# Performance work log

Measured on AMD Instinct MI355X. Metric: run time of the kernel, lower is better.

## Reference

```python
import jax, jax.numpy as jnp
import numpy as np

D = 1024  # encoder_output_size

def setup_inputs() -> dict:
    key = jax.random.key(0)
    ks = jax.random.split(key, 5)
    scale = 1.0 / np.sqrt(D)  # roughly matches nn.Linear init spread
    seq = jax.random.normal(ks[0], (2048, 8, D), dtype=jnp.float32)
    Kw1 = jax.random.normal(ks[1], (D, D), dtype=jnp.float32) * scale
    Kw2 = jax.random.normal(ks[2], (D, D), dtype=jnp.float32) * scale
    Qw1 = jax.random.normal(ks[3], (D, D), dtype=jnp.float32) * scale
    Qw2 = jax.random.normal(ks[4], (D, D), dtype=jnp.float32) * scale
    return {"sequence": seq, "Kw1": Kw1, "Kw2": Kw2, "Qw1": Qw1, "Qw2": Qw2}

def _mlp(x, W1, W2):
    # nn.Linear(bias=False): y = x @ W^T ; tanh after each
    return jnp.tanh(jnp.tanh(x @ W1.T) @ W2.T)

def reference(sequence, Kw1, Kw2, Qw1, Qw2):
    x = jnp.transpose(sequence, (1, 0, 2))          # [B, S, D]
    keys = _mlp(x, Kw1, Kw2)                        # [B, S, D]
    queries = _mlp(x, Qw1, Qw2)                     # [B, S, D]
    scale = 1.0 / jnp.sqrt(jnp.float32(x.shape[-1]))
    weights = jnp.einsum('bsd,btd->bst', keys, queries) * scale  # [B, S, S]
    weights = jax.nn.softmax(weights, axis=-1)
    attended = jnp.einsum('bst,btd->bsd', weights, x)            # [B, S, D]
    return jnp.transpose(attended, (1, 0, 2))       # [S, B, D]
```

## Files before the change

kernel.cpp:

```cpp
#include <hip/hip_runtime.h>
#include <hip/hip_bf16.h>

#define SEQ 2048
#define NB 8
#define DIM 1024

typedef __attribute__((ext_vector_type(4))) float f32x4;
typedef __attribute__((ext_vector_type(8))) short bf16x8;
typedef __attribute__((ext_vector_type(4))) unsigned short u16x4;

__device__ __forceinline__ unsigned short f2bf(float f) {
    union { float f; unsigned u; } x; x.f = f;
    unsigned r = x.u + 0x7fffu + ((x.u >> 16) & 1u);
    return (unsigned short)(r >> 16);
}
__device__ __forceinline__ float bf2f(unsigned short u) {
    union { unsigned u; float f; } x; x.u = ((unsigned)u) << 16;
    return x.f;
}

__global__ __launch_bounds__(256) void convert_w4(const float* __restrict__ s0,
                                                  const float* __restrict__ s1,
                                                  const float* __restrict__ s2,
                                                  const float* __restrict__ s3,
                                                  unsigned short* __restrict__ out) {
    int sel = blockIdx.y;
    const float* src = sel < 2 ? (sel == 0 ? s0 : s1) : (sel == 2 ? s2 : s3);
    int i = blockIdx.x * 256 + threadIdx.x;
    float4 v = reinterpret_cast<const float4*>(src)[i];
    u16x4 o = { f2bf(v.x), f2bf(v.y), f2bf(v.z), f2bf(v.w) };
    reinterpret_cast<u16x4*>(out + (size_t)sel * DIM * DIM)[i] = o;
}

__global__ __launch_bounds__(256) void make_xb(const float* __restrict__ seq,
                                               unsigned short* __restrict__ xb) {
    int sb = blockIdx.x;
    int s = sb >> 3, b = sb & 7;
    const float4* src = reinterpret_cast<const float4*>(seq + (size_t)sb * DIM);
    u16x4* dst = reinterpret_cast<u16x4*>(xb + ((size_t)b * SEQ + s) * DIM);
    int t = threadIdx.x;
    float4 v = src[t];
    u16x4 o = { f2bf(v.x), f2bf(v.y), f2bf(v.z), f2bf(v.w) };
    dst[t] = o;
}

__global__ __launch_bounds__(256) void make_xbT(const float* __restrict__ seq,
                                                unsigned short* __restrict__ xbT) {
    __shared__ unsigned short tile[64][65];
    int s0 = blockIdx.x * 64, d0 = blockIdx.y * 64, b = blockIdx.z;
    int t = threadIdx.x;
    int dx = (t & 15) * 4, sy = t >> 4;
    #pragma unroll
    for (int i = 0; i < 4; ++i) {
        int s = s0 + sy + i * 16;
        float4 v = *reinterpret_cast<const float4*>(seq + ((size_t)s * NB + b) * DIM + d0 + dx);
        tile[sy + i * 16][dx + 0] = f2bf(v.x);
        tile[sy + i * 16][dx + 1] = f2bf(v.y);
        tile[sy + i * 16][dx + 2] = f2bf(v.z);
        tile[sy + i * 16][dx + 3] = f2bf(v.w);
    }
    __syncthreads();
    int sx = (t & 15) * 4, dy = t >> 4;
    #pragma unroll
    for (int i = 0; i < 4; ++i) {
        int d = d0 + dy + i * 16;
        u16x4 o = { tile[sx + 0][dy + i * 16], tile[sx + 1][dy + i * 16],
                    tile[sx + 2][dy + i * 16], tile[sx + 3][dy + i * 16] };
        *reinterpret_cast<u16x4*>(xbT + ((size_t)b * DIM + d) * SEQ + s0 + sx) = o;
    }
}

__device__ __forceinline__ void gload16(const unsigned short* g, unsigned short* l) {
    __builtin_amdgcn_global_load_lds((const __attribute__((address_space(1))) void*)g,
                                     (__attribute__((address_space(3))) void*)l,
                                     16, 0, 0);
}

#define QUAD(A0, A1)                                                                              \
    _Pragma("unroll")                                                                             \
    for (int ks = 0; ks < 2; ++ks)                                                                \
        _Pragma("unroll")                                                                         \
        for (int ni = 0; ni < 4; ++ni) {                                                          \
            acc[A0][ni] = __builtin_amdgcn_mfma_f32_16x16x32_bf16(a[A0][ks], b[ni][ks], acc[A0][ni], 0, 0, 0); \
            acc[A1][ni] = __builtin_amdgcn_mfma_f32_16x16x32_bf16(a[A1][ks], b[ni][ks], acc[A1][ni], 0, 0, 0); \
        }

template<int MODE>
__global__ __launch_bounds__(512, 2) void gemm256(
    const unsigned short* __restrict__ A, size_t sA,
    const unsigned short* __restrict__ B, size_t sB,
    void* __restrict__ Cv, size_t sC,
    int ldc, int K, float scale)
{
    __shared__ unsigned short AsF[2 * 2 * 8192];
    __shared__ unsigned short BsF[2 * 2 * 8192];

    const int gx = gridDim.x, gy = gridDim.y;
    const int nwg = gx * gy * gridDim.z;
    const int fid = blockIdx.x + gx * (blockIdx.y + gy * blockIdx.z);
    const int cpx = nwg >> 3;
    const int sw = (fid & 7) * cpx + (fid >> 3);
    const int bx = sw % gx;
    const int rem = sw / gx;
    const int by = rem % gy;
    const int bz = rem / gy;

    const unsigned short* Ab = A + sA * bz;
    const unsigned short* Bb = B + sB * bz;
    const int m0 = by * 256;
    const int n0 = bx * 256;

    const int t_ = threadIdx.x;
    const int lane = t_ & 63;
    const int w = t_ >> 6;
    const int wm = w >> 2;
    const int wn = w & 3;

    const int l3 = lane >> 3;
    const int g7 = lane & 7;
    const size_t h128 = (size_t)128 * K;
    const size_t r8 = (size_t)8 * K;
    const unsigned short* gA = Ab + (size_t)(m0 + w * 16 + l3) * K + ((g7 ^ l3) << 3);
    const unsigned short* gB = Bb + (size_t)(n0 + w * 16 + l3) * K + ((g7 ^ l3) << 3);

    const int fr = lane & 15;
    const int hi4 = lane >> 4;
    const int off0 = fr * 64 + (((hi4) ^ g7) << 3);
    const int off1 = fr * 64 + (((4 + hi4) ^ g7) << 3);
    const int bno = (wn & 1) * 4096;
    const int wlds = w * 1024;

    f32x4 acc[8][4] = {};
    const int NT = K >> 6;

    #pragma unroll
    for (int kt = 0; kt < 2; ++kt) {
        unsigned short* lA = AsF + kt * 16384 + wlds;
        unsigned short* lB = BsF + kt * 16384 + wlds;
        const unsigned short* ga = gA + kt * 64;
        const unsigned short* gb = gB + kt * 64;
        gload16(ga, lA);                 gload16(ga + r8, lA + 512);
        gload16(ga + h128, lA + 8192);   gload16(ga + h128 + r8, lA + 8192 + 512);
        gload16(gb, lB);                 gload16(gb + r8, lB + 512);
        gload16(gb + h128, lB + 8192);   gload16(gb + h128 + r8, lB + 8192 + 512);
    }
    asm volatile("s_waitcnt vmcnt(8)" ::: "memory");
    __builtin_amdgcn_s_barrier();

    const unsigned short* gAs = gA + 128;
    const unsigned short* gBs = gB + 128;
    int bufo = 0;

    for (int t = 0; t < NT; ++t) {
        const unsigned short* pA = AsF + bufo + wm * 8192;
        const unsigned short* pB = BsF + bufo + (wn >> 1) * 8192 + bno;
        unsigned short* lA = AsF + bufo + wlds;
        unsigned short* lB = BsF + bufo + wlds;
        const bool pf = (t + 2 < NT);
        bf16x8 a[8][2], b[4][2];

        #pragma unroll
        for (int j = 0; j < 4; ++j) {
            b[j][0] = *(const bf16x8*)&pB[j * 1024 + off0];
            b[j][1] = *(const bf16x8*)&pB[j * 1024 + off1];
        }
        #pragma unroll
        for (int i = 0; i < 2; ++i) {
            a[i][0] = *(const bf16x8*)&pA[i * 1024 + off0];
            a[i][1] = *(const bf16x8*)&pA[i * 1024 + off1];
        }
        __builtin_amdgcn_s_barrier();
        asm volatile("s_waitcnt lgkmcnt(0)" ::: "memory");
        __builtin_amdgcn_sched_barrier(0);
        __builtin_amdgcn_s_setprio(1);
        QUAD(0, 1)
        __builtin_amdgcn_s_setprio(0);
        __builtin_amdgcn_s_barrier();

        #pragma unroll
        for (int i = 2; i < 4; ++i) {
            a[i][0] = *(const bf16x8*)&pA[i * 1024 + off0];
            a[i][1] = *(const bf16x8*)&pA[i * 1024 + off1];
        }
        if (pf) { gload16(gBs, lB); gload16(gBs + r8, lB + 512); }
        __builtin_amdgcn_s_barrier();
        asm volatile("s_waitcnt lgkmcnt(0)" ::: "memory");
        __builtin_amdgcn_sched_barrier(0);
        __builtin_amdgcn_s_setprio(1);
        QUAD(2, 3)
        __builtin_amdgcn_s_setprio(0);
        __builtin_amdgcn_s_barrier();

        #pragma unroll
        for (int i = 4; i < 8; ++i) {
            a[i][0] = *(const bf16x8*)&pA[i * 1024 + off0];
            a[i][1] = *(const bf16x8*)&pA[i * 1024 + off1];
        }
        if (pf) { gload16(gBs + h128, lB + 8192); gload16(gBs + h128 + r8, lB + 8192 + 512); }
        __builtin_amdgcn_s_barrier();
        asm volatile("s_waitcnt lgkmcnt(0)" ::: "memory");
        __builtin_amdgcn_sched_barrier(0);
        __builtin_amdgcn_s_setprio(1);
        QUAD(4, 5)
        __builtin_amdgcn_s_setprio(0);
        __builtin_amdgcn_s_barrier();

        if (pf) {
            gload16(gAs, lA);               gload16(gAs + r8, lA + 512);
            gload16(gAs + h128, lA + 8192); gload16(gAs + h128 + r8, lA + 8192 + 512);
            asm volatile("s_waitcnt vmcnt(8)" ::: "memory");
        } else {
            asm volatile("s_waitcnt vmcnt(0)" ::: "memory");
        }
        __builtin_amdgcn_s_barrier();
        __builtin_amdgcn_sched_barrier(0);
        __builtin_amdgcn_s_setprio(1);
        QUAD(6, 7)
        __builtin_amdgcn_s_setprio(0);
        __builtin_amdgcn_s_barrier();

        gAs += 64; gBs += 64; bufo ^= 16384;
    }

    #pragma unroll
    for (int mi = 0; mi < 8; ++mi)
        #pragma unroll
        for (int ni = 0; ni < 4; ++ni)
            #pragma unroll
            for (int r = 0; r < 4; ++r) {
                int row = m0 + wm * 128 + mi * 16 + hi4 * 4 + r;
                int col = n0 + wn * 64 + ni * 16 + fr;
                if (MODE == 0) {
                    unsigned short* C = reinterpret_cast<unsigned short*>(Cv);
                    C[(size_t)row * ldc + col] = f2bf(tanhf(acc[mi][ni][r]));
                } else if (MODE == 1) {
                    float* C = reinterpret_cast<float*>(Cv) + sC * bz;
                    C[(size_t)row * ldc + col] = acc[mi][ni][r] * scale;
                } else {
                    unsigned short* C = reinterpret_cast<unsigned short*>(Cv) + sC * bz;
                    C[(size_t)row * ldc + col] = f2bf(acc[mi][ni][r] * scale);
                }
            }
}

__global__ __launch_bounds__(256) void softmax_rows_bf16(unsigned short* __restrict__ Z) {
    const size_t row = blockIdx.x;
    unsigned short* z = Z + row * SEQ;
    const int t = threadIdx.x;
    u16x4 v0 = reinterpret_cast<const u16x4*>(z)[2 * t];
    u16x4 v1 = reinterpret_cast<const u16x4*>(z)[2 * t + 1];
    float f[8] = { bf2f(v0[0]), bf2f(v0[1]), bf2f(v0[2]), bf2f(v0[3]),
                   bf2f(v1[0]), bf2f(v1[1]), bf2f(v1[2]), bf2f(v1[3]) };
    float m = f[0];
    #pragma unroll
    for (int j = 1; j < 8; ++j) m = fmaxf(m, f[j]);
    #pragma unroll
    for (int off = 32; off; off >>= 1) m = fmaxf(m, __shfl_xor(m, off, 64));
    __shared__ float redm[4], reds[4];
    const int w = t >> 6, lane = t & 63;
    if (lane == 0) redm[w] = m;
    __syncthreads();
    m = fmaxf(fmaxf(redm[0], redm[1]), fmaxf(redm[2], redm[3]));
    float e[8], s = 0.f;
    #pragma unroll
    for (int j = 0; j < 8; ++j) { e[j] = __expf(f[j] - m); s += e[j]; }
    #pragma unroll
    for (int off = 32; off; off >>= 1) s += __shfl_xor(s, off, 64);
    if (lane == 0) reds[w] = s;
    __syncthreads();
    s = reds[0] + reds[1] + reds[2] + reds[3];
    float inv = 1.0f / s;
    u16x4 o0 = { f2bf(e[0] * inv), f2bf(e[1] * inv), f2bf(e[2] * inv), f2bf(e[3] * inv) };
    u16x4 o1 = { f2bf(e[4] * inv), f2bf(e[5] * inv), f2bf(e[6] * inv), f2bf(e[7] * inv) };
    reinterpret_cast<u16x4*>(z)[2 * t] = o0;
    reinterpret_cast<u16x4*>(z)[2 * t + 1] = o1;
}

extern "C" void kernel_launch(void* const* d_in, const int* in_sizes, int n_in,
                              void* d_out, int out_size, void* d_ws, size_t ws_size,
                              hipStream_t stream) {
    const float* seq  = (const float*)d_in[0];
    const float* Kw1f = (const float*)d_in[1];
    const float* Kw2f = (const float*)d_in[2];
    const float* Qw1f = (const float*)d_in[3];
    const float* Qw2f = (const float*)d_in[4];
    float* out = (float*)d_out;

    char* ws = (char*)d_ws;
    size_t off = 0;
    auto alloc = [&](size_t bytes) { void* p = ws + off; off += bytes; return p; };
    const size_t WBYTES = (size_t)DIM * DIM * 2;
    const size_t XBYTES = (size_t)NB * SEQ * DIM * 2;
    unsigned short* Wk1 = (unsigned short*)alloc(4 * WBYTES);
    unsigned short* Wk2 = Wk1 + (size_t)DIM * DIM;
    unsigned short* Wq1 = Wk2 + (size_t)DIM * DIM;
    unsigned short* Wq2 = Wq1 + (size_t)DIM * DIM;
    unsigned short* xb   = (unsigned short*)alloc(XBYTES);
    unsigned short* hbuf = (unsigned short*)alloc(XBYTES);
    unsigned short* keys = (unsigned short*)alloc(XBYTES);
    unsigned short* P    = (unsigned short*)alloc((size_t)NB * SEQ * SEQ * 2);
    unsigned short* qrs = xb;
    unsigned short* xbT = hbuf;

    convert_w4<<<dim3(DIM * DIM / 4 / 256, 4), 256, 0, stream>>>(Kw1f, Kw2f, Qw1f, Qw2f, Wk1);
    make_xb<<<SEQ * NB, 256, 0, stream>>>(seq, xb);

    dim3 gMLP(DIM / 256, (NB * SEQ) / 256, 1);
    gemm256<0><<<gMLP, 512, 0, stream>>>(xb,   0, Wk1, 0, hbuf, 0, DIM, DIM, 1.0f);
    gemm256<0><<<gMLP, 512, 0, stream>>>(hbuf, 0, Wk2, 0, keys, 0, DIM, DIM, 1.0f);
    gemm256<0><<<gMLP, 512, 0, stream>>>(xb,   0, Wq1, 0, hbuf, 0, DIM, DIM, 1.0f);
    gemm256<0><<<gMLP, 512, 0, stream>>>(hbuf, 0, Wq2, 0, qrs,  0, DIM, DIM, 1.0f);

    dim3 gQK(SEQ / 256, SEQ / 256, NB);
    gemm256<2><<<gQK, 512, 0, stream>>>(keys, (size_t)SEQ * DIM, qrs, (size_t)SEQ * DIM,
                                        P, (size_t)SEQ * SEQ, SEQ, DIM, 0.03125f);

    softmax_rows_bf16<<<NB * SEQ, 256, 0, stream>>>(P);

    make_xbT<<<dim3(SEQ / 64, DIM / 64, NB), 256, 0, stream>>>(seq, xbT);

    dim3 gPV(DIM / 256, SEQ / 256, NB);
    gemm256<1><<<gPV, 512, 0, stream>>>(P, (size_t)SEQ * SEQ, xbT, (size_t)DIM * SEQ,
                                        out, (size_t)DIM, NB * DIM, SEQ, 1.0f);
}
```

Before: 388.2 us.

## Restructure GEMM main loop into 4x2 quadrant MFMA order with staggered A/B prefetch

Reorders the 256x256 GEMM inner loop so each phase computes a 4x2 block of MFMA tiles (A rows 0-3 then 4-7, B columns 0-1 then 2-3) instead of pairs of A rows against all B columns. A is now prefetched one tile ahead into the opposite buffer while B is prefetched two tiles ahead into the current buffer, with adjusted vmcnt/lgkmcnt waits. The intent is to spread global-to-LDS loads across phases and to overlap LDS fragment reads with MFMA work. In exchange the buffer-reuse timing is more delicate and depends on barriers to avoid overwriting data still being read.

New measurement: 386.4 us. About the same (-0.5%).

```diff
diff --git a/kernel.cpp b/kernel.cpp
--- a/kernel.cpp
+++ b/kernel.cpp
@@ -76,14 +76,15 @@
                                      16, 0, 0);
 }
 
-#define QUAD(A0, A1)                                                                              \
+#define MFMA16(I0, J0)                                                                            \
     _Pragma("unroll")                                                                             \
     for (int ks = 0; ks < 2; ++ks)                                                                \
         _Pragma("unroll")                                                                         \
-        for (int ni = 0; ni < 4; ++ni) {                                                          \
-            acc[A0][ni] = __builtin_amdgcn_mfma_f32_16x16x32_bf16(a[A0][ks], b[ni][ks], acc[A0][ni], 0, 0, 0); \
-            acc[A1][ni] = __builtin_amdgcn_mfma_f32_16x16x32_bf16(a[A1][ks], b[ni][ks], acc[A1][ni], 0, 0, 0); \
-        }
+        for (int ii = 0; ii < 4; ++ii)                                                            \
+            _Pragma("unroll")                                                                     \
+            for (int jj = 0; jj < 2; ++jj)                                                        \
+                acc[I0 + ii][J0 + jj] = __builtin_amdgcn_mfma_f32_16x16x32_bf16(                   \
+                    a[I0 + ii][ks], b[J0 + jj][ks], acc[I0 + ii][J0 + jj], 0, 0, 0);
 
 template<int MODE>
 __global__ __launch_bounds__(512, 2) void gemm256(
@@ -133,61 +134,61 @@
     f32x4 acc[8][4] = {};
     const int NT = K >> 6;
 
-    #pragma unroll
-    for (int kt = 0; kt < 2; ++kt) {
-        unsigned short* lA = AsF + kt * 16384 + wlds;
-        unsigned short* lB = BsF + kt * 16384 + wlds;
-        const unsigned short* ga = gA + kt * 64;
-        const unsigned short* gb = gB + kt * 64;
-        gload16(ga, lA);                 gload16(ga + r8, lA + 512);
-        gload16(ga + h128, lA + 8192);   gload16(ga + h128 + r8, lA + 8192 + 512);
-        gload16(gb, lB);                 gload16(gb + r8, lB + 512);
-        gload16(gb + h128, lB + 8192);   gload16(gb + h128 + r8, lB + 8192 + 512);
+    gload16(gA, AsF + wlds);                    gload16(gA + r8, AsF + wlds + 512);
+    gload16(gA + h128, AsF + 8192 + wlds);      gload16(gA + h128 + r8, AsF + 8192 + wlds + 512);
+    gload16(gB, BsF + wlds);                    gload16(gB + r8, BsF + wlds + 512);
+    gload16(gB + h128, BsF + 8192 + wlds);      gload16(gB + h128 + r8, BsF + 8192 + wlds + 512);
+    {
+        const unsigned short* gb1 = gB + 64;
+        gload16(gb1, BsF + 16384 + wlds);               gload16(gb1 + r8, BsF + 16384 + wlds + 512);
+        gload16(gb1 + h128, BsF + 16384 + 8192 + wlds); gload16(gb1 + h128 + r8, BsF + 16384 + 8192 + wlds + 512);
     }
-    asm volatile("s_waitcnt vmcnt(8)" ::: "memory");
+    asm volatile("s_waitcnt vmcnt(4)" ::: "memory");
     __builtin_amdgcn_s_barrier();
 
-    const unsigned short* gAs = gA + 128;
-    const unsigned short* gBs = gB + 128;
-    int bufo = 0;
-
-    for (int t = 0; t < NT; ++t) {
-        const unsigned short* pA = AsF + bufo + wm * 8192;
-        const unsigned short* pB = BsF + bufo + (wn >> 1) * 8192 + bno;
-        unsigned short* lA = AsF + bufo + wlds;
-        unsigned short* lB = BsF + bufo + wlds;
-        const bool pf = (t + 2 < NT);
+    const unsigned short* gA1 = gA + 64;
+    const unsigned short* gB2 = gB + 128;
+
+    for (int u = 0; u < NT; ++u) {
+        const int bu = (u & 1) * 16384;
+        const int bn = 16384 - bu;
+        const unsigned short* pA = AsF + bu + wm * 8192;
+        const unsigned short* pB = BsF + bu + (wn >> 1) * 8192 + bno;
+        const bool pfA = (u + 1 < NT);
+        const bool pfB = (u + 2 < NT);
         bf16x8 a[8][2], b[4][2];
 
         #pragma unroll
-        for (int j = 0; j < 4; ++j) {
+        for (int i = 0; i < 4; ++i) {
+            a[i][0] = *(const bf16x8*)&pA[i * 1024 + off0];
+            a[i][1] = *(const bf16x8*)&pA[i * 1024 + off1];
+        }
+        #pragma unroll
+        for (int j = 0; j < 2; ++j) {
             b[j][0] = *(const bf16x8*)&pB[j * 1024 + off0];
             b[j][1] = *(const bf16x8*)&pB[j * 1024 + off1];
         }
-        #pragma unroll
-        for (int i = 0; i < 2; ++i) {
-            a[i][0] = *(const bf16x8*)&pA[i * 1024 + off0];
-            a[i][1] = *(const bf16x8*)&pA[i * 1024 + off1];
-        }
+        if (pfA) { gload16(gA1, AsF + bn + wlds); gload16(gA1 + r8, AsF + bn + wlds + 512); }
+        asm volatile("s_waitcnt lgkmcnt(8)" ::: "memory");
         __builtin_amdgcn_s_barrier();
         asm volatile("s_waitcnt lgkmcnt(0)" ::: "memory");
         __builtin_amdgcn_sched_barrier(0);
         __builtin_amdgcn_s_setprio(1);
-        QUAD(0, 1)
+        MFMA16(0, 0)
         __builtin_amdgcn_s_setprio(0);
         __builtin_amdgcn_s_barrier();
 
         #pragma unroll
-        for (int i = 2; i < 4; ++i) {
-            a[i][0] = *(const bf16x8*)&pA[i * 1024 + off0];
-            a[i][1] = *(const bf16x8*)&pA[i * 1024 + off1];
-        }
-        if (pf) { gload16(gBs, lB); gload16(gBs + r8, lB + 512); }
+        for (int j = 2; j < 4; ++j) {
+            b[j][0] = *(const bf16x8*)&pB[j * 1024 + off0];
+            b[j][1] = *(const bf16x8*)&pB[j * 1024 + off1];
+        }
+        if (pfA) { gload16(gA1 + h128, AsF + bn + 8192 + wlds); gload16(gA1 + h128 + r8, AsF + bn + 8192 + wlds + 512); }
         __builtin_amdgcn_s_barrier();
         asm volatile("s_waitcnt lgkmcnt(0)" ::: "memory");
         __builtin_amdgcn_sched_barrier(0);
         __builtin_amdgcn_s_setprio(1);
-        QUAD(2, 3)
+        MFMA16(0, 2)
         __builtin_amdgcn_s_setprio(0);
         __builtin_amdgcn_s_barrier();
 
@@ -196,30 +197,30 @@
             a[i][0] = *(const bf16x8*)&pA[i * 1024 + off0];
             a[i][1] = *(const bf16x8*)&pA[i * 1024 + off1];
         }
-        if (pf) { gload16(gBs + h128, lB + 8192); gload16(gBs + h128 + r8, lB + 8192 + 512); }
+        if (pfB) { gload16(gB2, BsF + bu + wlds); gload16(gB2 + r8, BsF + bu + wlds + 512); }
         __builtin_amdgcn_s_barrier();
         asm volatile("s_waitcnt lgkmcnt(0)" ::: "memory");
         __builtin_amdgcn_sched_barrier(0);
         __builtin_amdgcn_s_setprio(1);
-        QUAD(4, 5)
+        MFMA16(4, 0)
         __builtin_amdgcn_s_setprio(0);
         __builtin_amdgcn_s_barrier();
 
-        if (pf) {
-            gload16(gAs, lA);               gload16(gAs + r8, lA + 512);
-            gload16(gAs + h128, lA + 8192); gload16(gAs + h128 + r8, lA + 8192 + 512);
-            asm volatile("s_waitcnt vmcnt(8)" ::: "memory");
+        if (pfB) {
+            gload16(gB2 + h128, BsF + bu + 8192 + wlds);
+            gload16(gB2 + h128 + r8, BsF + bu + 8192 + wlds + 512);
+            asm volatile("s_waitcnt vmcnt(4)" ::: "memory");
         } else {
             asm volatile("s_waitcnt vmcnt(0)" ::: "memory");
         }
         __builtin_amdgcn_s_barrier();
         __builtin_amdgcn_sched_barrier(0);
         __builtin_amdgcn_s_setprio(1);
-        QUAD(6, 7)
+        MFMA16(4, 2)
         __builtin_amdgcn_s_setprio(0);
         __builtin_amdgcn_s_barrier();
 
-        gAs += 64; gBs += 64; bufo ^= 16384;
+        gA1 += 64; gB2 += 64;
     }
 
     #pragma unroll
```
